# Kernel tuning notes

Measured on AMD Instinct MI355X. Metric: run time of the kernel, lower is better.

Reference implementation:

```python
import jax, jax.numpy as jnp
import numpy as np

NT, NF, CIN, COUT = 1_500_000, 500_000, 32, 32
BN_EPS = 1e-5


def setup_inputs() -> dict:
    key = jax.random.key(0)
    k1, k2, k3 = jax.random.split(key, 3)
    input_texture = jax.random.normal(k1, (NT, CIN), dtype=jnp.float32)
    # barycentric coefficients: nonnegative, rows sum to 1
    b = jax.random.uniform(k2, (NT, 3), dtype=jnp.float32) + 1e-3
    bary_coeff = b / b.sum(axis=1, keepdims=True)
    # 3 texture samples per facet (sum == NT)
    num_texture = jnp.full((NF,), 3, dtype=jnp.int32)
    # xavier-normal init for [Cout, Cin, 3] kernel
    fan = CIN * 3 + COUT * 3
    std = float(np.sqrt(2.0 / fan))
    weights = jax.random.normal(k3, (COUT, CIN, 3), dtype=jnp.float32) * std
    bias = jnp.zeros((1, COUT), dtype=jnp.float32)
    gamma = jnp.ones((COUT,), dtype=jnp.float32)
    beta = jnp.zeros((COUT,), dtype=jnp.float32)
    return {"input_texture": input_texture, "bary_coeff": bary_coeff,
            "num_texture": num_texture, "weights": weights, "bias": bias,
            "gamma": gamma, "beta": beta}


def reference(input_texture, bary_coeff, num_texture, weights, bias, gamma, beta):
    nf = num_texture.shape[0]
    nt = input_texture.shape[0]
    # segment id for each ragged texture sample (original op uses cumsum offsets)
    seg = jnp.repeat(jnp.arange(nf), num_texture, total_repeat_length=nt)
    # per-sample contribution: y[t,o] = sum_{c,k} x[t,c] * b[t,k] * W[o,c,k]
    y = jnp.einsum('tc,tk,ock->to', input_texture, bary_coeff, weights)
    # facet2facet averages over the samples of each facet
    s = jax.ops.segment_sum(y, seg, num_segments=nf)  # [Nf, Cout]
    cnt = jnp.maximum(num_texture.astype(y.dtype), 1)[:, None]
    out = s / cnt
    out = out + bias          # bias add
    out = jax.nn.relu(out)    # activation
    # BatchNorm1d in training mode: batch statistics over the facet dim
    mean = out.mean(axis=0)
    var = out.var(axis=0)
    out = (out - mean) * jax.lax.rsqrt(var + BN_EPS) * gamma + beta
    return out
```

## Files before the change

### kernel.cpp

```cpp
#include <hip/hip_runtime.h>
#include <stdint.h>

typedef __attribute__((ext_vector_type(4))) float fv4;
typedef __attribute__((ext_vector_type(4))) short sv4;
typedef __attribute__((ext_vector_type(8))) short sv8;

#define SCHUNK 2048
#define FPB 128
#define PZB 108

static __device__ __forceinline__ short f2bf(float f) {
  union { float f; unsigned u; } v; v.f = f;
  unsigned u = v.u;
  u += 0x7fffu + ((u >> 16) & 1u);
  return (short)(u >> 16);
}

__global__ __launch_bounds__(256) void scan1(const int* __restrict__ num, int nf,
                                             int* __restrict__ bsum) {
  __shared__ int sd[256];
  int b = blockIdx.x, tid = threadIdx.x;
  int base = b * SCHUNK + tid * 8;
  int s = 0;
#pragma unroll
  for (int j = 0; j < 8; ++j) { int i = base + j; if (i < nf) s += num[i]; }
  sd[tid] = s; __syncthreads();
  for (int st = 128; st > 0; st >>= 1) {
    if (tid < st) sd[tid] += sd[tid + st];
    __syncthreads();
  }
  if (tid == 0) bsum[b] = sd[0];
}

__global__ __launch_bounds__(256) void scan2(int* __restrict__ bsum, int nb) {
  __shared__ int sd[256];
  int tid = threadIdx.x;
  int v = (tid < nb) ? bsum[tid] : 0;
  sd[tid] = v; __syncthreads();
  for (int off = 1; off < 256; off <<= 1) {
    int t = (tid >= off) ? sd[tid - off] : 0;
    __syncthreads();
    sd[tid] += t;
    __syncthreads();
  }
  if (tid < nb) bsum[tid] = sd[tid] - v;
}

__global__ __launch_bounds__(256) void scan3(const int* __restrict__ num, int nf,
                                             const int* __restrict__ bsum,
                                             int* __restrict__ offsets) {
  __shared__ int sc_[256];
  int b = blockIdx.x, tid = threadIdx.x;
  int base = b * SCHUNK + tid * 8;
  int loc[8]; int s = 0;
#pragma unroll
  for (int j = 0; j < 8; ++j) {
    loc[j] = (base + j < nf) ? num[base + j] : 0;
    s += loc[j];
  }
  sc_[tid] = s; __syncthreads();
  for (int off = 1; off < 256; off <<= 1) {
    int t = (tid >= off) ? sc_[tid - off] : 0;
    __syncthreads();
    sc_[tid] += t;
    __syncthreads();
  }
  int run = bsum[b] + sc_[tid] - s;
#pragma unroll
  for (int j = 0; j < 8; ++j) {
    if (base + j < nf) offsets[base + j] = run;
    run += loc[j];
  }
  if (b == gridDim.x - 1 && tid == 255) offsets[nf] = run;
}

__global__ __launch_bounds__(256) void k_main(
    const float* __restrict__ x, const float* __restrict__ bary,
    const float* __restrict__ W, const float* __restrict__ bias,
    const int* __restrict__ offsets, float* __restrict__ out,
    float* __restrict__ partials, int nf, int nblk)
{
  __shared__ short Z[FPB * PZB];
  __shared__ short W2[32 * PZB];
  __shared__ int off_s[FPB + 1];

  const int tid = threadIdx.x;
  const int f0 = blockIdx.x * FPB;

  for (int idx = tid; idx < 3072; idx += 256) {
    int o = idx / 96;
    int ck = idx - o * 96;
    int k = ck >> 5, c = ck & 31;
    W2[o * PZB + ck] = f2bf(W[o * 96 + c * 3 + k]);
  }
  for (int i = tid; i < FPB + 1; i += 256) {
    int f = f0 + i; if (f > nf) f = nf;
    off_s[i] = offsets[f];
  }
  __syncthreads();

  {
    const int fl = tid >> 1;
    const int cb = (tid & 1) * 16;
    const int st = off_s[fl], en = off_s[fl + 1];

    float z0[16], z1[16], z2[16];
#pragma unroll
    for (int j = 0; j < 16; ++j) { z0[j] = 0.f; z1[j] = 0.f; z2[j] = 0.f; }

    if (en - st == 3) {
      fv4 xs[3][4];
      float bb[3][3];
#pragma unroll
      for (int s = 0; s < 3; ++s) {
        const float* xp = x + (size_t)(st + s) * 32 + cb;
#pragma unroll
        for (int q = 0; q < 4; ++q) xs[s][q] = *(const fv4*)(xp + 4 * q);
      }
#pragma unroll
      for (int s = 0; s < 3; ++s) {
        const float* bp = bary + (size_t)(st + s) * 3;
        bb[s][0] = bp[0]; bb[s][1] = bp[1]; bb[s][2] = bp[2];
      }
#pragma unroll
      for (int s = 0; s < 3; ++s)
#pragma unroll
        for (int q = 0; q < 4; ++q)
#pragma unroll
          for (int j = 0; j < 4; ++j) {
            float xv = xs[s][q][j];
            z0[q * 4 + j] += xv * bb[s][0];
            z1[q * 4 + j] += xv * bb[s][1];
            z2[q * 4 + j] += xv * bb[s][2];
          }
    } else {
      for (int t = st; t < en; ++t) {
        const float* xp = x + (size_t)t * 32 + cb;
        fv4 xa = *(const fv4*)(xp);
        fv4 xb = *(const fv4*)(xp + 4);
        fv4 xc = *(const fv4*)(xp + 8);
        fv4 xd = *(const fv4*)(xp + 12);
        const float* bp = bary + (size_t)t * 3;
        float b0 = bp[0], b1 = bp[1], b2 = bp[2];
#pragma unroll
        for (int j = 0; j < 4; ++j) {
          z0[j]      += xa[j] * b0; z1[j]      += xa[j] * b1; z2[j]      += xa[j] * b2;
          z0[4 + j]  += xb[j] * b0; z1[4 + j]  += xb[j] * b1; z2[4 + j]  += xb[j] * b2;
          z0[8 + j]  += xc[j] * b0; z1[8 + j]  += xc[j] * b1; z2[8 + j]  += xc[j] * b2;
          z0[12 + j] += xd[j] * b0; z1[12 + j] += xd[j] * b1; z2[12 + j] += xd[j] * b2;
        }
      }
    }

    short* zr = &Z[fl * PZB + cb];
#pragma unroll
    for (int g = 0; g < 4; ++g) {
      sv4 p0, p1, p2;
#pragma unroll
      for (int j = 0; j < 4; ++j) {
        p0[j] = f2bf(z0[g * 4 + j]);
        p1[j] = f2bf(z1[g * 4 + j]);
        p2[j] = f2bf(z2[g * 4 + j]);
      }
      *(sv4*)(zr + g * 4)      = p0;
      *(sv4*)(zr + 32 + g * 4) = p1;
      *(sv4*)(zr + 64 + g * 4) = p2;
    }
  }
  __syncthreads();

  const int lane = tid & 63;
  const int wv = tid >> 6;
  const int rowl = lane & 15;
  const int grp = lane >> 4;

  fv4 acc[2][2];
#pragma unroll
  for (int m = 0; m < 2; ++m)
#pragma unroll
    for (int n = 0; n < 2; ++n)
      acc[m][n] = (fv4){0.f, 0.f, 0.f, 0.f};

#pragma unroll
  for (int kb = 0; kb < 3; ++kb) {
    const int cko = kb * 32 + grp * 4;
    sv8 bfr[2];
#pragma unroll
    for (int n = 0; n < 2; ++n) {
      const short* wr = &W2[(n * 16 + rowl) * PZB + cko];
      sv4 lo = *(const sv4*)(wr);
      sv4 hi = *(const sv4*)(wr + 16);
#pragma unroll
      for (int j = 0; j < 4; ++j) { bfr[n][j] = lo[j]; bfr[n][4 + j] = hi[j]; }
    }
#pragma unroll
    for (int m = 0; m < 2; ++m) {
      const short* zr = &Z[(wv * 32 + m * 16 + rowl) * PZB + cko];
      sv4 lo = *(const sv4*)(zr);
      sv4 hi = *(const sv4*)(zr + 16);
      sv8 afr;
#pragma unroll
      for (int j = 0; j < 4; ++j) { afr[j] = lo[j]; afr[4 + j] = hi[j]; }
      acc[m][0] = __builtin_amdgcn_mfma_f32_16x16x32_bf16(afr, bfr[0], acc[m][0], 0, 0, 0);
      acc[m][1] = __builtin_amdgcn_mfma_f32_16x16x32_bf16(afr, bfr[1], acc[m][1], 0, 0, 0);
    }
  }
  __syncthreads();

  float* yt = (float*)Z;
#pragma unroll
  for (int m = 0; m < 2; ++m)
#pragma unroll
    for (int n = 0; n < 2; ++n)
#pragma unroll
      for (int r = 0; r < 4; ++r)
        yt[(wv * 32 + m * 16 + grp * 4 + r) * 33 + n * 16 + rowl] = acc[m][n][r];
  __syncthreads();

  const int o_ep = tid & 31;
  const int g_ep = tid >> 5;
  float bo = bias[o_ep];
  float s1 = 0.f, s2 = 0.f;
#pragma unroll
  for (int i = 0; i < 16; ++i) {
    int fl = i * 8 + g_ep;
    int f = f0 + fl;
    if (f < nf) {
      int nm = off_s[fl + 1] - off_s[fl];
      float v = yt[fl * 33 + o_ep] / (float)(nm > 1 ? nm : 1) + bo;
      v = fmaxf(v, 0.f);
      out[f * 32 + o_ep] = v;
      s1 += v; s2 += v * v;
    }
  }
  __syncthreads();
  float* red = (float*)W2;
  red[tid] = s1;
  red[256 + tid] = s2;
  __syncthreads();
  if (tid < 32) {
    float a1 = 0.f, a2 = 0.f;
#pragma unroll
    for (int g = 0; g < 8; ++g) { a1 += red[g * 32 + tid]; a2 += red[256 + g * 32 + tid]; }
    partials[(long)tid * nblk + blockIdx.x]        = a1;
    partials[(long)(32 + tid) * nblk + blockIdx.x] = a2;
  }
}

__global__ __launch_bounds__(256) void k_reduce(const float* __restrict__ partials,
                                                int nblk, float* __restrict__ stats) {
  __shared__ float sd[256];
  int c = blockIdx.x;
  const float* p = partials + (long)c * nblk;
  float s = 0.f;
  for (int i = threadIdx.x; i < nblk; i += 256) s += p[i];
  sd[threadIdx.x] = s; __syncthreads();
  for (int st = 128; st > 0; st >>= 1) {
    if (threadIdx.x < st) sd[threadIdx.x] += sd[threadIdx.x + st];
    __syncthreads();
  }
  if (threadIdx.x == 0) stats[c] = sd[0];
}

__global__ __launch_bounds__(256) void k_bn(float* __restrict__ out,
                                            const float* __restrict__ stats,
                                            const float* __restrict__ gamma,
                                            const float* __restrict__ beta, int nf) {
  __shared__ float sc[32], sh[32];
  if (threadIdx.x < 32) {
    int o = threadIdx.x;
    float inv_n = 1.0f / (float)nf;
    float mean = stats[o] * inv_n;
    float var = stats[32 + o] * inv_n - mean * mean;
    float rstd = rsqrtf(var + 1e-5f);
    float g = gamma[o] * rstd;
    sc[o] = g;
    sh[o] = beta[o] - mean * g;
  }
  __syncthreads();
  long total4 = (long)nf * 8;
  long idx0 = (long)blockIdx.x * 256 + threadIdx.x;
  int ob = ((int)idx0 & 7) * 4;
  fv4 scv = *(const fv4*)&sc[ob];
  fv4 shv = *(const fv4*)&sh[ob];
  for (long idx = idx0; idx < total4; idx += (long)gridDim.x * 256) {
    fv4 v = *((const fv4*)out + idx);
    v = v * scv + shv;
    *((fv4*)out + idx) = v;
  }
}

extern "C" void kernel_launch(void* const* d_in, const int* in_sizes, int n_in,
                              void* d_out, int out_size, void* d_ws, size_t ws_size,
                              hipStream_t stream) {
  const float* x     = (const float*)d_in[0];
  const float* bary  = (const float*)d_in[1];
  const int*   numt  = (const int*)d_in[2];
  const float* W     = (const float*)d_in[3];
  const float* bias  = (const float*)d_in[4];
  const float* gamma = (const float*)d_in[5];
  const float* beta  = (const float*)d_in[6];
  float* out = (float*)d_out;

  const int nf   = in_sizes[2];
  const int nblk = (nf + FPB - 1) / FPB;
  const int nbS  = (nf + SCHUNK - 1) / SCHUNK;

  char* w = (char*)d_ws;
  int* offsets = (int*)w;
  size_t off1 = (4UL * (size_t)(nf + 1) + 255) & ~255UL;
  int* bsum = (int*)(w + off1);
  size_t off2 = (off1 + 4UL * (size_t)nbS + 255) & ~255UL;
  float* partials = (float*)(w + off2);
  size_t off3 = (off2 + 4UL * 64UL * (size_t)nblk + 255) & ~255UL;
  float* stats = (float*)(w + off3);

  scan1<<<nbS, 256, 0, stream>>>(numt, nf, bsum);
  scan2<<<1, 256, 0, stream>>>(bsum, nbS);
  scan3<<<nbS, 256, 0, stream>>>(numt, nf, bsum, offsets);
  k_main<<<nblk, 256, 0, stream>>>(x, bary, W, bias, offsets, out, partials, nf, nblk);
  k_reduce<<<64, 256, 0, stream>>>(partials, nblk, stats);
  k_bn<<<2048, 256, 0, stream>>>(out, stats, gamma, beta, nf);
}
```

Measured before the change: 112.7 us.

## Halve facets per block and split channels across four threads per facet

Reduces facets per block from 128 to 64, so each thread now handles 8 channels of one facet (4 threads per facet) and each wave does a single 16-row MFMA tile. The grid doubles, which aims to raise occupancy and memory-level parallelism and cut per-thread register use. The cost is more blocks writing partial BN statistics, more redundant per-block weight conversion into LDS, and narrower global loads per thread. The bf16 conversion also switches to the HIP intrinsic.

Measured after the change: 109.8 us. -2.6%, faster.

```diff
diff --git a/kernel.cpp b/kernel.cpp
--- a/kernel.cpp
+++ b/kernel.cpp
@@ -1,4 +1,5 @@
 #include <hip/hip_runtime.h>
+#include <hip/hip_bf16.h>
 #include <stdint.h>
 
 typedef __attribute__((ext_vector_type(4))) float fv4;
@@ -6,14 +7,13 @@
 typedef __attribute__((ext_vector_type(8))) short sv8;
 
 #define SCHUNK 2048
-#define FPB 128
+#define FPB 64
 #define PZB 108
 
 static __device__ __forceinline__ short f2bf(float f) {
-  union { float f; unsigned u; } v; v.f = f;
-  unsigned u = v.u;
-  u += 0x7fffu + ((u >> 16) & 1u);
-  return (short)(u >> 16);
+  __hip_bfloat16 h = __float2bfloat16(f);
+  union { __hip_bfloat16 h; short s; } u; u.h = h;
+  return u.s;
 }
 
 __global__ __launch_bounds__(256) void scan1(const int* __restrict__ num, int nf,
@@ -93,29 +93,29 @@
     int k = ck >> 5, c = ck & 31;
     W2[o * PZB + ck] = f2bf(W[o * 96 + c * 3 + k]);
   }
-  for (int i = tid; i < FPB + 1; i += 256) {
-    int f = f0 + i; if (f > nf) f = nf;
-    off_s[i] = offsets[f];
+  if (tid < FPB + 1) {
+    int f = f0 + tid; if (f > nf) f = nf;
+    off_s[tid] = offsets[f];
   }
   __syncthreads();
 
   {
-    const int fl = tid >> 1;
-    const int cb = (tid & 1) * 16;
+    const int fl = tid >> 2;
+    const int cb = (tid & 3) * 8;
     const int st = off_s[fl], en = off_s[fl + 1];
 
-    float z0[16], z1[16], z2[16];
-#pragma unroll
-    for (int j = 0; j < 16; ++j) { z0[j] = 0.f; z1[j] = 0.f; z2[j] = 0.f; }
+    float z0[8], z1[8], z2[8];
+#pragma unroll
+    for (int j = 0; j < 8; ++j) { z0[j] = 0.f; z1[j] = 0.f; z2[j] = 0.f; }
 
     if (en - st == 3) {
-      fv4 xs[3][4];
+      fv4 xs[3][2];
       float bb[3][3];
 #pragma unroll
       for (int s = 0; s < 3; ++s) {
         const float* xp = x + (size_t)(st + s) * 32 + cb;
-#pragma unroll
-        for (int q = 0; q < 4; ++q) xs[s][q] = *(const fv4*)(xp + 4 * q);
+        xs[s][0] = *(const fv4*)(xp);
+        xs[s][1] = *(const fv4*)(xp + 4);
       }
 #pragma unroll
       for (int s = 0; s < 3; ++s) {
@@ -125,7 +125,7 @@
 #pragma unroll
       for (int s = 0; s < 3; ++s)
 #pragma unroll
-        for (int q = 0; q < 4; ++q)
+        for (int q = 0; q < 2; ++q)
 #pragma unroll
           for (int j = 0; j < 4; ++j) {
             float xv = xs[s][q][j];
@@ -138,23 +138,19 @@
         const float* xp = x + (size_t)t * 32 + cb;
         fv4 xa = *(const fv4*)(xp);
         fv4 xb = *(const fv4*)(xp + 4);
-        fv4 xc = *(const fv4*)(xp + 8);
-        fv4 xd = *(const fv4*)(xp + 12);
         const float* bp = bary + (size_t)t * 3;
         float b0 = bp[0], b1 = bp[1], b2 = bp[2];
 #pragma unroll
         for (int j = 0; j < 4; ++j) {
-          z0[j]      += xa[j] * b0; z1[j]      += xa[j] * b1; z2[j]      += xa[j] * b2;
-          z0[4 + j]  += xb[j] * b0; z1[4 + j]  += xb[j] * b1; z2[4 + j]  += xb[j] * b2;
-          z0[8 + j]  += xc[j] * b0; z1[8 + j]  += xc[j] * b1; z2[8 + j]  += xc[j] * b2;
-          z0[12 + j] += xd[j] * b0; z1[12 + j] += xd[j] * b1; z2[12 + j] += xd[j] * b2;
+          z0[j]     += xa[j] * b0; z1[j]     += xa[j] * b1; z2[j]     += xa[j] * b2;
+          z0[4 + j] += xb[j] * b0; z1[4 + j] += xb[j] * b1; z2[4 + j] += xb[j] * b2;
         }
       }
     }
 
     short* zr = &Z[fl * PZB + cb];
 #pragma unroll
-    for (int g = 0; g < 4; ++g) {
+    for (int g = 0; g < 2; ++g) {
       sv4 p0, p1, p2;
 #pragma unroll
       for (int j = 0; j < 4; ++j) {
@@ -174,12 +170,9 @@
   const int rowl = lane & 15;
   const int grp = lane >> 4;
 
-  fv4 acc[2][2];
-#pragma unroll
-  for (int m = 0; m < 2; ++m)
-#pragma unroll
-    for (int n = 0; n < 2; ++n)
-      acc[m][n] = (fv4){0.f, 0.f, 0.f, 0.f};
+  fv4 acc[2];
+  acc[0] = (fv4){0.f, 0.f, 0.f, 0.f};
+  acc[1] = (fv4){0.f, 0.f, 0.f, 0.f};
 
 #pragma unroll
   for (int kb = 0; kb < 3; ++kb) {
@@ -193,28 +186,23 @@
 #pragma unroll
       for (int j = 0; j < 4; ++j) { bfr[n][j] = lo[j]; bfr[n][4 + j] = hi[j]; }
     }
-#pragma unroll
-    for (int m = 0; m < 2; ++m) {
-      const short* zr = &Z[(wv * 32 + m * 16 + rowl) * PZB + cko];
-      sv4 lo = *(const sv4*)(zr);
-      sv4 hi = *(const sv4*)(zr + 16);
-      sv8 afr;
-#pragma unroll
-      for (int j = 0; j < 4; ++j) { afr[j] = lo[j]; afr[4 + j] = hi[j]; }
-      acc[m][0] = __builtin_amdgcn_mfma_f32_16x16x32_bf16(afr, bfr[0], acc[m][0], 0, 0, 0);
-      acc[m][1] = __builtin_amdgcn_mfma_f32_16x16x32_bf16(afr, bfr[1], acc[m][1], 0, 0, 0);
-    }
+    const short* zr = &Z[(wv * 16 + rowl) * PZB + cko];
+    sv4 lo = *(const sv4*)(zr);
+    sv4 hi = *(const sv4*)(zr + 16);
+    sv8 afr;
+#pragma unroll
+    for (int j = 0; j < 4; ++j) { afr[j] = lo[j]; afr[4 + j] = hi[j]; }
+    acc[0] = __builtin_amdgcn_mfma_f32_16x16x32_bf16(afr, bfr[0], acc[0], 0, 0, 0);
+    acc[1] = __builtin_amdgcn_mfma_f32_16x16x32_bf16(afr, bfr[1], acc[1], 0, 0, 0);
   }
   __syncthreads();
 
   float* yt = (float*)Z;
 #pragma unroll
-  for (int m = 0; m < 2; ++m)
-#pragma unroll
-    for (int n = 0; n < 2; ++n)
-#pragma unroll
-      for (int r = 0; r < 4; ++r)
-        yt[(wv * 32 + m * 16 + grp * 4 + r) * 33 + n * 16 + rowl] = acc[m][n][r];
+  for (int n = 0; n < 2; ++n)
+#pragma unroll
+    for (int r = 0; r < 4; ++r)
+      yt[(wv * 16 + grp * 4 + r) * 33 + n * 16 + rowl] = acc[n][r];
   __syncthreads();
 
   const int o_ep = tid & 31;
@@ -222,7 +210,7 @@
   float bo = bias[o_ep];
   float s1 = 0.f, s2 = 0.f;
 #pragma unroll
-  for (int i = 0; i < 16; ++i) {
+  for (int i = 0; i < 8; ++i) {
     int fl = i * 8 + g_ep;
     int f = f0 + fl;
     if (f < nf) {
```
